# Performance work log

Measured on AMD Instinct MI355X. Metric: run time of the kernel, lower is better.

## Reference

```python
import jax, jax.numpy as jnp
import numpy as np
import math

EMB = 100

def setup_inputs() -> dict:
    key = jax.random.key(0)
    ks = jax.random.split(key, 10)
    B, L = 4, 512
    src = jax.random.normal(ks[0], (B, L, EMB), dtype=jnp.float32)
    att_w = jnp.ones((3,), dtype=jnp.float32)
    conv_w1 = jax.random.normal(ks[1], (10, 1, 1, EMB), dtype=jnp.float32) * 0.05
    conv_b1 = jax.random.normal(ks[2], (10,), dtype=jnp.float32) * 0.05
    conv_w2 = jax.random.normal(ks[3], (10, 1, 2, EMB), dtype=jnp.float32) * 0.05
    conv_b2 = jax.random.normal(ks[4], (10,), dtype=jnp.float32) * 0.05
    conv_w3 = jax.random.normal(ks[5], (10, 1, 3, EMB), dtype=jnp.float32) * 0.05
    conv_b3 = jax.random.normal(ks[6], (10,), dtype=jnp.float32) * 0.05
    lin_w = jax.random.normal(ks[7], (30, 2), dtype=jnp.float32) * 0.05
    lin_b = jax.random.normal(ks[8], (2,), dtype=jnp.float32) * 0.05
    return {"src": src, "att_w": att_w,
            "conv_w1": conv_w1, "conv_b1": conv_b1,
            "conv_w2": conv_w2, "conv_b2": conv_b2,
            "conv_w3": conv_w3, "conv_b3": conv_b3,
            "lin_w": lin_w, "lin_b": lin_b}

def _dot_attention(x):
    # [B,L,L] scores, softmax over keys, weighted sum
    scores = jnp.einsum('bqd,bkd->bqk', x, x)
    return jnp.einsum('bqk,bkd->bqd', jax.nn.softmax(scores, axis=-1), x)

def _scaled_dot_attention(q, k, v):
    d_k = k.shape[-1]
    scores = jnp.einsum('bqd,bkd->bqk', q, k) / math.sqrt(d_k)
    return jnp.einsum('bqk,bkd->bqd', jax.nn.softmax(scores, axis=-1), v)

def _additive_attention(q, k, v):
    # explicit O(L^2 * d) broadcast as in the original module
    scores = jnp.tanh(q[:, :, None, :] + k[:, None, :, :]).sum(axis=-1)  # [B,L,L]
    return jnp.einsum('bqk,bkd->bqd', jax.nn.softmax(scores, axis=-1), v)

def _conv_branch(x, w, b, ws):
    # x: [B,1,L,EMB], w: [10,1,ws,EMB]; torch padding=(ws-1, 0) pads both sides in H
    y = jax.lax.conv_general_dilated(
        x, w, window_strides=(1, 1),
        padding=[(ws - 1, ws - 1), (0, 0)],
        dimension_numbers=('NCHW', 'OIHW', 'NCHW'))
    y = jax.nn.relu(y + b[None, :, None, None])  # [B,10,L+ws-1,1]
    return jnp.max(y[..., 0], axis=2)            # global max-pool over time -> [B,10]

def reference(src, att_w, conv_w1, conv_b1, conv_w2, conv_b2, conv_w3, conv_b3, lin_w, lin_b):
    a1 = _dot_attention(src)
    a2 = _additive_attention(src, src, src)
    a3 = _scaled_dot_attention(src, src, src)
    w = att_w / att_w.sum()
    attn = w[0] * a1 + w[1] * a2 + w[2] * a3
    x = (src + attn)[:, None, :, :]  # [B,1,L,EMB]
    pooled = jnp.concatenate([
        _conv_branch(x, conv_w1, conv_b1, 1),
        _conv_branch(x, conv_w2, conv_b2, 2),
        _conv_branch(x, conv_w3, conv_b3, 3),
    ], axis=1)  # [B,30]; dropout is identity in eval mode
    return pooled @ lin_w + lin_b
```

## Files before the change

### kernel.cpp

```cpp
#include <hip/hip_runtime.h>

#define B_ 4
#define L_ 512
#define D_ 100

__device__ __forceinline__ float fexp2(float x) { return __builtin_amdgcn_exp2f(x); }
__device__ __forceinline__ float frcp(float x)  { return __builtin_amdgcn_rcpf(x); }

__global__ __launch_bounds__(256) void k_scores(const float* __restrict__ x,
                                                float* __restrict__ E1,
                                                float* __restrict__ E2,
                                                float* __restrict__ E3,
                                                float* __restrict__ Zp) {
  const int kt = blockIdx.x, qt = blockIdx.y, b = blockIdx.z;
  if (kt < qt) return;
  __shared__ float2 XQ[32 * 101];
  __shared__ float2 XK[32 * 101];
  __shared__ float colred[4][16][6];
  const float C = 2.8853900817779268f;
  const float L2E = 1.4426950408889634f;
  const float* xb = x + (size_t)b * L_ * D_;
  const int tid = threadIdx.x;
  for (int i = tid; i < 32 * D_; i += 256) {
    int r = i / D_, c = i - r * D_;
    float xq = xb[(qt * 32 + r) * D_ + c];
    float xk = xb[(kt * 32 + r) * D_ + c];
    XQ[r * 101 + c] = make_float2(xq, fexp2(xq * C));
    XK[r * 101 + c] = make_float2(xk, fexp2(xk * C));
  }
  __syncthreads();
  const int tx = tid & 15, ty = tid >> 4;
  float s00 = 0, s01 = 0, s10 = 0, s11 = 0;
  float r00 = 0, r01 = 0, r10 = 0, r11 = 0;
  const float2* qp0 = &XQ[ty * 101];
  const float2* qp1 = &XQ[(ty + 16) * 101];
  const float2* kp0 = &XK[tx * 101];
  const float2* kp1 = &XK[(tx + 16) * 101];
#pragma unroll 4
  for (int d = 0; d < D_; ++d) {
    float2 a0 = qp0[d], a1 = qp1[d], b0 = kp0[d], b1 = kp1[d];
    s00 += a0.x * b0.x; s01 += a0.x * b1.x; s10 += a1.x * b0.x; s11 += a1.x * b1.x;
    r00 += frcp(fmaf(a0.y, b0.y, 1.0f));
    r01 += frcp(fmaf(a0.y, b1.y, 1.0f));
    r10 += frcp(fmaf(a1.y, b0.y, 1.0f));
    r11 += frcp(fmaf(a1.y, b1.y, 1.0f));
  }
  float t00 = (float)D_ - 2.0f * r00;
  float t01 = (float)D_ - 2.0f * r01;
  float t10 = (float)D_ - 2.0f * r10;
  float t11 = (float)D_ - 2.0f * r11;
  float e1_00 = fexp2(fmaf(s00, L2E, -120.0f)), e1_01 = fexp2(fmaf(s01, L2E, -120.0f));
  float e1_10 = fexp2(fmaf(s10, L2E, -120.0f)), e1_11 = fexp2(fmaf(s11, L2E, -120.0f));
  float e2_00 = fexp2(fmaf(t00, L2E, -32.0f)),  e2_01 = fexp2(fmaf(t01, L2E, -32.0f));
  float e2_10 = fexp2(fmaf(t10, L2E, -32.0f)),  e2_11 = fexp2(fmaf(t11, L2E, -32.0f));
  const float L2E10 = 0.14426950408889634f;
  float e3_00 = fexp2(s00 * L2E10), e3_01 = fexp2(s01 * L2E10);
  float e3_10 = fexp2(s10 * L2E10), e3_11 = fexp2(s11 * L2E10);

  const int q0r = qt * 32 + ty, q1r = q0r + 16;
  const int k0 = kt * 32 + tx, k1 = k0 + 16;
  float* E1b = E1 + (size_t)b * L_ * L_;
  float* E2b = E2 + (size_t)b * L_ * L_;
  float* E3b = E3 + (size_t)b * L_ * L_;
  E1b[q0r * L_ + k0] = e1_00; E1b[q0r * L_ + k1] = e1_01;
  E1b[q1r * L_ + k0] = e1_10; E1b[q1r * L_ + k1] = e1_11;
  E2b[q0r * L_ + k0] = e2_00; E2b[q0r * L_ + k1] = e2_01;
  E2b[q1r * L_ + k0] = e2_10; E2b[q1r * L_ + k1] = e2_11;
  E3b[q0r * L_ + k0] = e3_00; E3b[q0r * L_ + k1] = e3_01;
  E3b[q1r * L_ + k0] = e3_10; E3b[q1r * L_ + k1] = e3_11;
  if (kt != qt) {
    E1b[k0 * L_ + q0r] = e1_00; E1b[k1 * L_ + q0r] = e1_01;
    E1b[k0 * L_ + q1r] = e1_10; E1b[k1 * L_ + q1r] = e1_11;
    E2b[k0 * L_ + q0r] = e2_00; E2b[k1 * L_ + q0r] = e2_01;
    E2b[k0 * L_ + q1r] = e2_10; E2b[k1 * L_ + q1r] = e2_11;
    E3b[k0 * L_ + q0r] = e3_00; E3b[k1 * L_ + q0r] = e3_01;
    E3b[k0 * L_ + q1r] = e3_10; E3b[k1 * L_ + q1r] = e3_11;
  }

  float rs[3][2];
  rs[0][0] = e1_00 + e1_01; rs[0][1] = e1_10 + e1_11;
  rs[1][0] = e2_00 + e2_01; rs[1][1] = e2_10 + e2_11;
  rs[2][0] = e3_00 + e3_01; rs[2][1] = e3_10 + e3_11;
#pragma unroll
  for (int o = 8; o > 0; o >>= 1) {
#pragma unroll
    for (int e = 0; e < 3; ++e) {
      rs[e][0] += __shfl_xor(rs[e][0], o);
      rs[e][1] += __shfl_xor(rs[e][1], o);
    }
  }
  if (tx == 0) {
#pragma unroll
    for (int e = 0; e < 3; ++e) {
      Zp[(((size_t)b * L_ + q0r) * 16 + kt) * 3 + e] = rs[e][0];
      Zp[(((size_t)b * L_ + q1r) * 16 + kt) * 3 + e] = rs[e][1];
    }
  }

  float cs_[3][2];
  cs_[0][0] = e1_00 + e1_10; cs_[0][1] = e1_01 + e1_11;
  cs_[1][0] = e2_00 + e2_10; cs_[1][1] = e2_01 + e2_11;
  cs_[2][0] = e3_00 + e3_10; cs_[2][1] = e3_01 + e3_11;
#pragma unroll
  for (int o = 16; o <= 32; o <<= 1) {
#pragma unroll
    for (int e = 0; e < 3; ++e) {
      cs_[e][0] += __shfl_xor(cs_[e][0], o);
      cs_[e][1] += __shfl_xor(cs_[e][1], o);
    }
  }
  const int wv = tid >> 6, lane = tid & 63;
  if ((lane >> 4) == 0) {
#pragma unroll
    for (int e = 0; e < 3; ++e) {
      colred[wv][tx][e * 2 + 0] = cs_[e][0];
      colred[wv][tx][e * 2 + 1] = cs_[e][1];
    }
  }
  __syncthreads();
  if (kt != qt && tid < 96) {
    int txx = tid / 6, j = tid - txx * 6;
    float v = colred[0][txx][j] + colred[1][txx][j] + colred[2][txx][j] + colred[3][txx][j];
    int e = j >> 1, half = j & 1;
    int krow = kt * 32 + txx + half * 16;
    Zp[(((size_t)b * L_ + krow) * 16 + qt) * 3 + e] = v;
  }
}

__global__ __launch_bounds__(256) void k_pv(const float* __restrict__ x,
    const float* __restrict__ E1, const float* __restrict__ E2,
    const float* __restrict__ E3, const float* __restrict__ Zp,
    const float* __restrict__ attw,
    float* __restrict__ Xp, float* __restrict__ pooled) {
  const int qg = blockIdx.x, ks = blockIdx.y, b = blockIdx.z;
  const int tid = threadIdx.x;
  if (qg == 0 && ks == 0 && b == 0 && tid < B_ * 30) pooled[tid] = 0.0f;
  __shared__ float cs[8][3];
  __shared__ float P[8][128];
  const int q0 = qg * 8;
  if (tid < 24) {
    int row = tid / 3, j = tid - row * 3;
    const float* zp = Zp + (((size_t)b * L_ + q0 + row) * 16) * 3 + j;
    float z = 0.0f;
#pragma unroll
    for (int t = 0; t < 16; ++t) z += zp[t * 3];
    float winv = frcp(attw[0] + attw[1] + attw[2]);
    cs[row][j] = attw[j] * winv * frcp(z);
  }
  __syncthreads();
  for (int idx = tid; idx < 8 * 128; idx += 256) {
    int row = idx >> 7, kk = idx & 127;
    size_t o = ((size_t)b * L_ + q0 + row) * (size_t)L_ + ks * 128 + kk;
    P[row][kk] = cs[row][0] * E1[o] + cs[row][1] * E2[o] + cs[row][2] * E3[o];
  }
  __syncthreads();
  const int d = tid & 127, qh = tid >> 7;
  if (d >= D_) return;
  const float* xb = x + (size_t)b * L_ * D_ + (size_t)(ks * 128) * D_;
  const int r0 = qh * 4;
  float a0 = 0, a1 = 0, a2 = 0, a3 = 0;
  for (int kk = 0; kk < 128; kk += 4) {
    float4 p0 = *(const float4*)&P[r0 + 0][kk];
    float4 p1 = *(const float4*)&P[r0 + 1][kk];
    float4 p2 = *(const float4*)&P[r0 + 2][kk];
    float4 p3 = *(const float4*)&P[r0 + 3][kk];
    float x0 = xb[(kk + 0) * D_ + d];
    float x1 = xb[(kk + 1) * D_ + d];
    float x2 = xb[(kk + 2) * D_ + d];
    float x3 = xb[(kk + 3) * D_ + d];
    a0 += p0.x * x0 + p0.y * x1 + p0.z * x2 + p0.w * x3;
    a1 += p1.x * x0 + p1.y * x1 + p1.z * x2 + p1.w * x3;
    a2 += p2.x * x0 + p2.y * x1 + p2.z * x2 + p2.w * x3;
    a3 += p3.x * x0 + p3.y * x1 + p3.z * x2 + p3.w * x3;
  }
  size_t o = (((size_t)ks * B_ + b) * L_ + q0 + r0) * D_ + d;
  Xp[o]          = a0;
  Xp[o + D_]     = a1;
  Xp[o + 2 * D_] = a2;
  Xp[o + 3 * D_] = a3;
}

__global__ __launch_bounds__(256) void k_conv(const float* __restrict__ src,
    const float* __restrict__ Xp,
    const float* __restrict__ w1, const float* __restrict__ b1,
    const float* __restrict__ w2, const float* __restrict__ b2,
    const float* __restrict__ w3, const float* __restrict__ b3,
    float* __restrict__ pooled) {
  const int tt = blockIdx.x, cg = blockIdx.y, b = blockIdx.z;
  __shared__ float xs[66 * 101];
  __shared__ float wl[8][300];
  const int tid = threadIdx.x;
  const float* xb  = src + (size_t)b * L_ * D_;
  const float* pp0 = Xp + ((size_t)(0 * B_ + b) * L_) * D_;
  const float* pp1 = Xp + ((size_t)(1 * B_ + b) * L_) * D_;
  const float* pp2 = Xp + ((size_t)(2 * B_ + b) * L_) * D_;
  const float* pp3 = Xp + ((size_t)(3 * B_ + b) * L_) * D_;
  const int t0 = tt * 64;
  for (int i = tid; i < 66 * D_; i += 256) {
    int r = i / D_, c = i - r * D_;
    int rg = t0 - 2 + r;
    float v = 0.0f;
    if (rg >= 0 && rg < L_) {
      size_t o = (size_t)rg * D_ + c;
      v = xb[o] + pp0[o] + pp1[o] + pp2[o] + pp3[o];
    }
    xs[r * 101 + c] = v;
  }
  for (int i = tid; i < 8 * 300; i += 256) {
    int cl = i / 300, rest = i - cl * 300;
    int h = rest / D_, dd = rest - h * D_;
    int c = cg * 8 + cl;
    float wv = 0.0f;
    if (c < 30) {
      int ws = 1 + c / 10;
      int hh = h - (3 - ws);
      if (hh >= 0) {
        if (ws == 1)      wv = w1[c * D_ + dd];
        else if (ws == 2) wv = w2[(c - 10) * 2 * D_ + hh * D_ + dd];
        else              wv = w3[(c - 20) * 3 * D_ + hh * D_ + dd];
      }
    }
    wl[cl][h * D_ + dd] = wv;
  }
  __syncthreads();
  const int tl = tid & 63, g = tid >> 6;
  const int tg = t0 + tl;
  const int cl0 = g, cl1 = g + 4;
  float acc0 = 0, acc1 = 0;
#pragma unroll
  for (int h = 0; h < 3; ++h) {
#pragma unroll 4
    for (int dd = 0; dd < D_; ++dd) {
      float xv = xs[(tl + h) * 101 + dd];
      acc0 += xv * wl[cl0][h * D_ + dd];
      acc1 += xv * wl[cl1][h * D_ + dd];
    }
  }
#pragma unroll
  for (int j = 0; j < 2; ++j) {
    int c = cg * 8 + (j == 0 ? cl0 : cl1);
    float acc = (j == 0) ? acc0 : acc1;
    if (c < 30) {
      int ws = 1 + c / 10;
      float bias = (ws == 1) ? b1[c] : (ws == 2 ? b2[c - 10] : b3[c - 20]);
      float v = (tg < L_ + ws - 1) ? fmaxf(acc + bias, 0.0f) : 0.0f;
#pragma unroll
      for (int o = 32; o > 0; o >>= 1) v = fmaxf(v, __shfl_xor(v, o));
      if (tl == 0)
        atomicMax(reinterpret_cast<int*>(&pooled[b * 30 + c]), __float_as_int(v));
    }
  }
}

__global__ void k_linear(const float* __restrict__ pooled,
                         const float* __restrict__ lw,
                         const float* __restrict__ lb,
                         float* __restrict__ out) {
  int i = threadIdx.x;
  if (i >= B_ * 2) return;
  int b = i >> 1, j = i & 1;
  float acc = lb[j];
#pragma unroll
  for (int c = 0; c < 30; ++c) acc += pooled[b * 30 + c] * lw[c * 2 + j];
  out[b * 2 + j] = acc;
}

extern "C" void kernel_launch(void* const* d_in, const int* in_sizes, int n_in,
                              void* d_out, int out_size, void* d_ws, size_t ws_size,
                              hipStream_t stream) {
  const float* src  = (const float*)d_in[0];
  const float* attw = (const float*)d_in[1];
  const float* w1   = (const float*)d_in[2];
  const float* b1   = (const float*)d_in[3];
  const float* w2   = (const float*)d_in[4];
  const float* b2   = (const float*)d_in[5];
  const float* w3   = (const float*)d_in[6];
  const float* b3   = (const float*)d_in[7];
  const float* lw   = (const float*)d_in[8];
  const float* lb   = (const float*)d_in[9];

  float* E1 = (float*)d_ws;
  float* E2 = E1 + (size_t)B_ * L_ * L_;
  float* E3 = E2 + (size_t)B_ * L_ * L_;
  float* Zp = E3 + (size_t)B_ * L_ * L_;
  float* Xp = Zp + (size_t)B_ * L_ * 16 * 3;
  float* PL = Xp + (size_t)4 * B_ * L_ * D_;
  float* out = (float*)d_out;

  hipLaunchKernelGGL(k_scores, dim3(16, 16, B_), dim3(256), 0, stream, src, E1, E2, E3, Zp);
  hipLaunchKernelGGL(k_pv,     dim3(64, 4, B_),  dim3(256), 0, stream, src, E1, E2, E3, Zp, attw, Xp, PL);
  hipLaunchKernelGGL(k_conv,   dim3(9, 4, B_),   dim3(256), 0, stream, src, Xp, w1, b1, w2, b2, w3, b3, PL);
  hipLaunchKernelGGL(k_linear, dim3(1), dim3(64), 0, stream, PL, lw, lb, out);
}
```

Measured before the change: 68.08 us.

## Compact triangular grid, coalesce mirrored stores, fuse PV split-K reduction and linear

The scores kernel now launches only the upper-triangular tiles via a linear index, pads LDS rows to allow float4 reads, and writes the mirrored E tiles through an LDS transpose so the global stores are coalesced. The PV kernel uses 1024-thread blocks that reduce all four key splits in LDS and add the residual, so the conv kernel reads a single X2 array instead of summing five. The final linear layer is folded into the conv kernel using an atomic counter that lets the last block finish, which removes one launch. This adds extra syncs, larger blocks that may lower occupancy, and a last-block pattern that depends on a counter reset done in the first kernel.

New measurement: 58.79 us. -13.6%, faster.

```diff
diff --git a/kernel.cpp b/kernel.cpp
--- a/kernel.cpp
+++ b/kernel.cpp
@@ -11,39 +11,54 @@
                                                 float* __restrict__ E1,
                                                 float* __restrict__ E2,
                                                 float* __restrict__ E3,
-                                                float* __restrict__ Zp) {
-  const int kt = blockIdx.x, qt = blockIdx.y, b = blockIdx.z;
-  if (kt < qt) return;
-  __shared__ float2 XQ[32 * 101];
-  __shared__ float2 XK[32 * 101];
+                                                float* __restrict__ Zp,
+                                                int* __restrict__ counter,
+                                                float* __restrict__ pooled) {
+  const int b = blockIdx.y;
+  const int tid = threadIdx.x;
+  if (blockIdx.x == 0 && b == 0) {
+    if (tid < B_ * 30) pooled[tid] = 0.0f;
+    if (tid == 128) *counter = 0;
+  }
+  int qt = 0, rem = blockIdx.x;
+  while (rem >= 16 - qt) { rem -= (16 - qt); ++qt; }
+  const int kt = qt + rem;
+
+  __shared__ float2 XQ[32 * 102];
+  __shared__ float2 XK[32 * 102];
   __shared__ float colred[4][16][6];
   const float C = 2.8853900817779268f;
   const float L2E = 1.4426950408889634f;
   const float* xb = x + (size_t)b * L_ * D_;
-  const int tid = threadIdx.x;
   for (int i = tid; i < 32 * D_; i += 256) {
     int r = i / D_, c = i - r * D_;
     float xq = xb[(qt * 32 + r) * D_ + c];
     float xk = xb[(kt * 32 + r) * D_ + c];
-    XQ[r * 101 + c] = make_float2(xq, fexp2(xq * C));
-    XK[r * 101 + c] = make_float2(xk, fexp2(xk * C));
+    XQ[r * 102 + c] = make_float2(xq, fexp2(xq * C));
+    XK[r * 102 + c] = make_float2(xk, fexp2(xk * C));
   }
   __syncthreads();
   const int tx = tid & 15, ty = tid >> 4;
   float s00 = 0, s01 = 0, s10 = 0, s11 = 0;
   float r00 = 0, r01 = 0, r10 = 0, r11 = 0;
-  const float2* qp0 = &XQ[ty * 101];
-  const float2* qp1 = &XQ[(ty + 16) * 101];
-  const float2* kp0 = &XK[tx * 101];
-  const float2* kp1 = &XK[(tx + 16) * 101];
-#pragma unroll 4
-  for (int d = 0; d < D_; ++d) {
-    float2 a0 = qp0[d], a1 = qp1[d], b0 = kp0[d], b1 = kp1[d];
-    s00 += a0.x * b0.x; s01 += a0.x * b1.x; s10 += a1.x * b0.x; s11 += a1.x * b1.x;
-    r00 += frcp(fmaf(a0.y, b0.y, 1.0f));
-    r01 += frcp(fmaf(a0.y, b1.y, 1.0f));
-    r10 += frcp(fmaf(a1.y, b0.y, 1.0f));
-    r11 += frcp(fmaf(a1.y, b1.y, 1.0f));
+  const float2* qp0 = &XQ[ty * 102];
+  const float2* qp1 = &XQ[(ty + 16) * 102];
+  const float2* kp0 = &XK[tx * 102];
+  const float2* kp1 = &XK[(tx + 16) * 102];
+#pragma unroll 2
+  for (int d = 0; d < D_; d += 2) {
+    float4 A0 = *(const float4*)&qp0[d];
+    float4 A1 = *(const float4*)&qp1[d];
+    float4 B0 = *(const float4*)&kp0[d];
+    float4 B1 = *(const float4*)&kp1[d];
+    s00 += A0.x * B0.x + A0.z * B0.z;
+    s01 += A0.x * B1.x + A0.z * B1.z;
+    s10 += A1.x * B0.x + A1.z * B0.z;
+    s11 += A1.x * B1.x + A1.z * B1.z;
+    r00 += frcp(fmaf(A0.y, B0.y, 1.0f)) + frcp(fmaf(A0.w, B0.w, 1.0f));
+    r01 += frcp(fmaf(A0.y, B1.y, 1.0f)) + frcp(fmaf(A0.w, B1.w, 1.0f));
+    r10 += frcp(fmaf(A1.y, B0.y, 1.0f)) + frcp(fmaf(A1.w, B0.w, 1.0f));
+    r11 += frcp(fmaf(A1.y, B1.y, 1.0f)) + frcp(fmaf(A1.w, B1.w, 1.0f));
   }
   float t00 = (float)D_ - 2.0f * r00;
   float t01 = (float)D_ - 2.0f * r01;
@@ -68,14 +83,6 @@
   E2b[q1r * L_ + k0] = e2_10; E2b[q1r * L_ + k1] = e2_11;
   E3b[q0r * L_ + k0] = e3_00; E3b[q0r * L_ + k1] = e3_01;
   E3b[q1r * L_ + k0] = e3_10; E3b[q1r * L_ + k1] = e3_11;
-  if (kt != qt) {
-    E1b[k0 * L_ + q0r] = e1_00; E1b[k1 * L_ + q0r] = e1_01;
-    E1b[k0 * L_ + q1r] = e1_10; E1b[k1 * L_ + q1r] = e1_11;
-    E2b[k0 * L_ + q0r] = e2_00; E2b[k1 * L_ + q0r] = e2_01;
-    E2b[k0 * L_ + q1r] = e2_10; E2b[k1 * L_ + q1r] = e2_11;
-    E3b[k0 * L_ + q0r] = e3_00; E3b[k1 * L_ + q0r] = e3_01;
-    E3b[k0 * L_ + q1r] = e3_10; E3b[k1 * L_ + q1r] = e3_11;
-  }
 
   float rs[3][2];
   rs[0][0] = e1_00 + e1_01; rs[0][1] = e1_10 + e1_11;
@@ -118,25 +125,53 @@
     }
   }
   __syncthreads();
-  if (kt != qt && tid < 96) {
-    int txx = tid / 6, j = tid - txx * 6;
-    float v = colred[0][txx][j] + colred[1][txx][j] + colred[2][txx][j] + colred[3][txx][j];
-    int e = j >> 1, half = j & 1;
-    int krow = kt * 32 + txx + half * 16;
-    Zp[(((size_t)b * L_ + krow) * 16 + qt) * 3 + e] = v;
+  if (kt != qt) {
+    if (tid < 96) {
+      int txx = tid / 6, j = tid - txx * 6;
+      float v = colred[0][txx][j] + colred[1][txx][j] + colred[2][txx][j] + colred[3][txx][j];
+      int e = j >> 1, half = j & 1;
+      int krow = kt * 32 + txx + half * 16;
+      Zp[(((size_t)b * L_ + krow) * 16 + qt) * 3 + e] = v;
+    }
+    float* M = (float*)XK;
+    const int mo = ty * 33 + tx;
+    M[mo] = e1_00; M[mo + 16] = e1_01;
+    M[mo + 16 * 33] = e1_10; M[mo + 16 * 33 + 16] = e1_11;
+    __syncthreads();
+#pragma unroll
+    for (int j = 0; j < 4; ++j) {
+      int idx = tid + 256 * j, kr = idx >> 5, qc = idx & 31;
+      E1b[(kt * 32 + kr) * L_ + qt * 32 + qc] = M[qc * 33 + kr];
+    }
+    __syncthreads();
+    M[mo] = e2_00; M[mo + 16] = e2_01;
+    M[mo + 16 * 33] = e2_10; M[mo + 16 * 33 + 16] = e2_11;
+    __syncthreads();
+#pragma unroll
+    for (int j = 0; j < 4; ++j) {
+      int idx = tid + 256 * j, kr = idx >> 5, qc = idx & 31;
+      E2b[(kt * 32 + kr) * L_ + qt * 32 + qc] = M[qc * 33 + kr];
+    }
+    __syncthreads();
+    M[mo] = e3_00; M[mo + 16] = e3_01;
+    M[mo + 16 * 33] = e3_10; M[mo + 16 * 33 + 16] = e3_11;
+    __syncthreads();
+#pragma unroll
+    for (int j = 0; j < 4; ++j) {
+      int idx = tid + 256 * j, kr = idx >> 5, qc = idx & 31;
+      E3b[(kt * 32 + kr) * L_ + qt * 32 + qc] = M[qc * 33 + kr];
+    }
   }
 }
 
-__global__ __launch_bounds__(256) void k_pv(const float* __restrict__ x,
+__global__ __launch_bounds__(1024) void k_pv(const float* __restrict__ x,
     const float* __restrict__ E1, const float* __restrict__ E2,
     const float* __restrict__ E3, const float* __restrict__ Zp,
-    const float* __restrict__ attw,
-    float* __restrict__ Xp, float* __restrict__ pooled) {
-  const int qg = blockIdx.x, ks = blockIdx.y, b = blockIdx.z;
+    const float* __restrict__ attw, float* __restrict__ X2) {
+  const int qg = blockIdx.x, b = blockIdx.y;
   const int tid = threadIdx.x;
-  if (qg == 0 && ks == 0 && b == 0 && tid < B_ * 30) pooled[tid] = 0.0f;
   __shared__ float cs[8][3];
-  __shared__ float P[8][128];
+  __shared__ float P[8][512];
   const int q0 = qg * 8;
   if (tid < 24) {
     int row = tid / 3, j = tid - row * 3;
@@ -148,63 +183,67 @@
     cs[row][j] = attw[j] * winv * frcp(z);
   }
   __syncthreads();
-  for (int idx = tid; idx < 8 * 128; idx += 256) {
-    int row = idx >> 7, kk = idx & 127;
-    size_t o = ((size_t)b * L_ + q0 + row) * (size_t)L_ + ks * 128 + kk;
+  for (int idx = tid; idx < 8 * 512; idx += 1024) {
+    int row = idx >> 9, kk = idx & 511;
+    size_t o = ((size_t)b * L_ + q0 + row) * (size_t)L_ + kk;
     P[row][kk] = cs[row][0] * E1[o] + cs[row][1] * E2[o] + cs[row][2] * E3[o];
   }
   __syncthreads();
-  const int d = tid & 127, qh = tid >> 7;
-  if (d >= D_) return;
-  const float* xb = x + (size_t)b * L_ * D_ + (size_t)(ks * 128) * D_;
+  const int d = tid & 127, ks = (tid >> 7) & 3, qh = tid >> 9;
   const int r0 = qh * 4;
   float a0 = 0, a1 = 0, a2 = 0, a3 = 0;
-  for (int kk = 0; kk < 128; kk += 4) {
-    float4 p0 = *(const float4*)&P[r0 + 0][kk];
-    float4 p1 = *(const float4*)&P[r0 + 1][kk];
-    float4 p2 = *(const float4*)&P[r0 + 2][kk];
-    float4 p3 = *(const float4*)&P[r0 + 3][kk];
-    float x0 = xb[(kk + 0) * D_ + d];
-    float x1 = xb[(kk + 1) * D_ + d];
-    float x2 = xb[(kk + 2) * D_ + d];
-    float x3 = xb[(kk + 3) * D_ + d];
-    a0 += p0.x * x0 + p0.y * x1 + p0.z * x2 + p0.w * x3;
-    a1 += p1.x * x0 + p1.y * x1 + p1.z * x2 + p1.w * x3;
-    a2 += p2.x * x0 + p2.y * x1 + p2.z * x2 + p2.w * x3;
-    a3 += p3.x * x0 + p3.y * x1 + p3.z * x2 + p3.w * x3;
-  }
-  size_t o = (((size_t)ks * B_ + b) * L_ + q0 + r0) * D_ + d;
-  Xp[o]          = a0;
-  Xp[o + D_]     = a1;
-  Xp[o + 2 * D_] = a2;
-  Xp[o + 3 * D_] = a3;
+  if (d < D_) {
+    const float* xb = x + (size_t)b * L_ * D_ + (size_t)(ks * 128) * D_;
+    const int kb = ks * 128;
+    for (int kk = 0; kk < 128; kk += 4) {
+      float4 p0 = *(const float4*)&P[r0 + 0][kb + kk];
+      float4 p1 = *(const float4*)&P[r0 + 1][kb + kk];
+      float4 p2 = *(const float4*)&P[r0 + 2][kb + kk];
+      float4 p3 = *(const float4*)&P[r0 + 3][kb + kk];
+      float x0 = xb[(kk + 0) * D_ + d];
+      float x1 = xb[(kk + 1) * D_ + d];
+      float x2 = xb[(kk + 2) * D_ + d];
+      float x3 = xb[(kk + 3) * D_ + d];
+      a0 += p0.x * x0 + p0.y * x1 + p0.z * x2 + p0.w * x3;
+      a1 += p1.x * x0 + p1.y * x1 + p1.z * x2 + p1.w * x3;
+      a2 += p2.x * x0 + p2.y * x1 + p2.z * x2 + p2.w * x3;
+      a3 += p3.x * x0 + p3.y * x1 + p3.z * x2 + p3.w * x3;
+    }
+  }
+  __syncthreads();
+  float* R = &P[0][0];
+  R[((ks * 8) + r0 + 0) * 128 + d] = a0;
+  R[((ks * 8) + r0 + 1) * 128 + d] = a1;
+  R[((ks * 8) + r0 + 2) * 128 + d] = a2;
+  R[((ks * 8) + r0 + 3) * 128 + d] = a3;
+  __syncthreads();
+  if (tid < 8 * D_) {
+    int row = tid / D_, dd = tid - row * D_;
+    float v = R[(0 * 8 + row) * 128 + dd] + R[(1 * 8 + row) * 128 + dd] +
+              R[(2 * 8 + row) * 128 + dd] + R[(3 * 8 + row) * 128 + dd];
+    size_t o = ((size_t)b * L_ + q0 + row) * D_ + dd;
+    X2[o] = x[o] + v;
+  }
 }
 
-__global__ __launch_bounds__(256) void k_conv(const float* __restrict__ src,
-    const float* __restrict__ Xp,
+__global__ __launch_bounds__(256) void k_conv(const float* __restrict__ X2,
     const float* __restrict__ w1, const float* __restrict__ b1,
     const float* __restrict__ w2, const float* __restrict__ b2,
     const float* __restrict__ w3, const float* __restrict__ b3,
-    float* __restrict__ pooled) {
+    const float* __restrict__ lw, const float* __restrict__ lb,
+    float* __restrict__ pooled, int* __restrict__ counter,
+    float* __restrict__ out) {
   const int tt = blockIdx.x, cg = blockIdx.y, b = blockIdx.z;
   __shared__ float xs[66 * 101];
   __shared__ float wl[8][300];
+  __shared__ int lastFlag;
   const int tid = threadIdx.x;
-  const float* xb  = src + (size_t)b * L_ * D_;
-  const float* pp0 = Xp + ((size_t)(0 * B_ + b) * L_) * D_;
-  const float* pp1 = Xp + ((size_t)(1 * B_ + b) * L_) * D_;
-  const float* pp2 = Xp + ((size_t)(2 * B_ + b) * L_) * D_;
-  const float* pp3 = Xp + ((size_t)(3 * B_ + b) * L_) * D_;
+  const float* xb = X2 + (size_t)b * L_ * D_;
   const int t0 = tt * 64;
   for (int i = tid; i < 66 * D_; i += 256) {
     int r = i / D_, c = i - r * D_;
     int rg = t0 - 2 + r;
-    float v = 0.0f;
-    if (rg >= 0 && rg < L_) {
-      size_t o = (size_t)rg * D_ + c;
-      v = xb[o] + pp0[o] + pp1[o] + pp2[o] + pp3[o];
-    }
-    xs[r * 101 + c] = v;
+    xs[r * 101 + c] = (rg >= 0 && rg < L_) ? xb[(size_t)rg * D_ + c] : 0.0f;
   }
   for (int i = tid; i < 8 * 300; i += 256) {
     int cl = i / 300, rest = i - cl * 300;
@@ -250,19 +289,24 @@
         atomicMax(reinterpret_cast<int*>(&pooled[b * 30 + c]), __float_as_int(v));
     }
   }
-}
-
-__global__ void k_linear(const float* __restrict__ pooled,
-                         const float* __restrict__ lw,
-                         const float* __restrict__ lb,
-                         float* __restrict__ out) {
-  int i = threadIdx.x;
-  if (i >= B_ * 2) return;
-  int b = i >> 1, j = i & 1;
-  float acc = lb[j];
-#pragma unroll
-  for (int c = 0; c < 30; ++c) acc += pooled[b * 30 + c] * lw[c * 2 + j];
-  out[b * 2 + j] = acc;
+  __syncthreads();
+  if (tid == 0) {
+    __threadfence();
+    int old = atomicAdd(counter, 1);
+    lastFlag = (old == 9 * 4 * B_ - 1);
+  }
+  __syncthreads();
+  if (lastFlag && tid < B_ * 2) {
+    int bb = tid >> 1, j = tid & 1;
+    float acc = lb[j];
+    int* pI = reinterpret_cast<int*>(pooled);
+#pragma unroll
+    for (int c = 0; c < 30; ++c) {
+      int pi = atomicMax(&pI[bb * 30 + c], 0);
+      acc = fmaf(__int_as_float(pi), lw[c * 2 + j], acc);
+    }
+    out[bb * 2 + j] = acc;
+  }
 }
 
 extern "C" void kernel_launch(void* const* d_in, const int* in_sizes, int n_in,
@@ -283,12 +327,15 @@
   float* E2 = E1 + (size_t)B_ * L_ * L_;
   float* E3 = E2 + (size_t)B_ * L_ * L_;
   float* Zp = E3 + (size_t)B_ * L_ * L_;
-  float* Xp = Zp + (size_t)B_ * L_ * 16 * 3;
-  float* PL = Xp + (size_t)4 * B_ * L_ * D_;
+  float* X2 = Zp + (size_t)B_ * L_ * 16 * 3;
+  float* PL = X2 + (size_t)B_ * L_ * D_;
+  int* counter = (int*)(PL + 128);
   float* out = (float*)d_out;
 
-  hipLaunchKernelGGL(k_scores, dim3(16, 16, B_), dim3(256), 0, stream, src, E1, E2, E3, Zp);
-  hipLaunchKernelGGL(k_pv,     dim3(64, 4, B_),  dim3(256), 0, stream, src, E1, E2, E3, Zp, attw, Xp, PL);
-  hipLaunchKernelGGL(k_conv,   dim3(9, 4, B_),   dim3(256), 0, stream, src, Xp, w1, b1, w2, b2, w3, b3, PL);
-  hipLaunchKernelGGL(k_linear, dim3(1), dim3(64), 0, stream, PL, lw, lb, out);
+  hipLaunchKernelGGL(k_scores, dim3(136, B_), dim3(256), 0, stream,
+                     src, E1, E2, E3, Zp, counter, PL);
+  hipLaunchKernelGGL(k_pv, dim3(L_ / 8, B_), dim3(1024), 0, stream,
+                     src, E1, E2, E3, Zp, attw, X2);
+  hipLaunchKernelGGL(k_conv, dim3(9, 4, B_), dim3(256), 0, stream,
+                     X2, w1, b1, w2, b2, w3, b3, lw, lb, PL, counter, out);
 }
```
